# Kernel optimization log

Measured on AMD Instinct MI355X. Metric: run time of the kernel, lower is better.

The kernel has to match this reference:

```python
import jax, jax.numpy as jnp
import numpy as np

B = 16          # frames in batch
N = 16384       # atoms (num_nodes)
R = 1024        # residues (segments)
D = 320         # input_dim
BINS = 32       # adaptive-pool feature bins (output_size_per_segment[1])
H = 512         # mlp_hidden_dim
COND = 3        # conditioner dim (X_ref)
EPS = 1e-5


def setup_inputs() -> dict:
    key = jax.random.key(0)
    ks = jax.random.split(key, 8)
    x = jax.random.normal(ks[0], (B * N, D), dtype=jnp.float32)
    cond = jax.random.normal(ks[1], (N, COND), dtype=jnp.float32)
    # sorted residue ids -> contiguous variable-size segments, like real residues
    seg_ids = jnp.sort(jax.random.randint(ks[2], (N,), 0, R, dtype=jnp.int32))
    W1 = jax.random.normal(ks[3], (BINS + COND, H), dtype=jnp.float32) * 0.05
    b1 = jnp.zeros((H,), jnp.float32)
    gamma = jnp.ones((H,), jnp.float32)
    beta = jnp.zeros((H,), jnp.float32)
    bn_mean = jnp.zeros((H,), jnp.float32)
    bn_var = jnp.ones((H,), jnp.float32)
    W2 = jax.random.normal(ks[4], (H, 3), dtype=jnp.float32) * 0.05
    b2 = jnp.zeros((3,), jnp.float32)
    return {"x": x, "cond": cond, "seg_ids": seg_ids, "W1": W1, "b1": b1,
            "gamma": gamma, "beta": beta, "bn_mean": bn_mean, "bn_var": bn_var,
            "W2": W2, "b2": b2}


def reference(x, cond, seg_ids, W1, b1, gamma, beta, bn_mean, bn_var, W2, b2):
    # x: [B*N, D] atom embeddings
    x3 = x.reshape(B, N, D)
    # --- per-residue AdaptiveAvgPool2d((1, BINS)) as a fused segment mean ---
    # output height 1 == mean over all atoms of the residue
    counts = jax.ops.segment_sum(jnp.ones((N,), x.dtype), seg_ids, num_segments=R)
    sums = jax.vmap(lambda xb: jax.ops.segment_sum(xb, seg_ids, num_segments=R))(x3)  # [B,R,D]
    seg_mean = sums / jnp.maximum(counts, 1.0)[None, :, None]
    # adaptive width D -> BINS (D divisible by BINS => exact chunk means)
    pooled = seg_mean.reshape(B, R, BINS, D // BINS).mean(-1)  # [B,R,BINS]
    # --- broadcast residue feature back to atoms, concat conditioner ---
    per_atom = pooled[:, seg_ids, :]                           # [B,N,BINS]
    cond_b = jnp.broadcast_to(cond[None], (B, N, COND))
    feat = jnp.concatenate([per_atom, cond_b], axis=-1).reshape(B * N, BINS + COND)
    # --- decoder MLP: Linear -> ReLU -> BatchNorm1d(eval) -> Linear ---
    h = jnp.maximum(feat @ W1 + b1, 0.0)
    h = (h - bn_mean) * jax.lax.rsqrt(bn_var + EPS) * gamma + beta
    out = h @ W2 + b2                                          # [B*N, 3]
    return out
```

## Files before the change

### kernel.cpp

```cpp
#include <hip/hip_runtime.h>
#include <math.h>

#define B_ 16
#define N_ 16384
#define R_ 1024
#define D_ 320
#define BINS_ 32
#define H_ 512
#define EPS_ 1e-5f
#define AP 516
#define EP 260

__global__ void k_segoff(const int* __restrict__ seg, int* __restrict__ off){
  int g = blockIdx.x * blockDim.x + threadIdx.x;
  if (g > R_) return;
  int lo = 0, hi = N_;
  while (lo < hi){ int mid = (lo + hi) >> 1; if (seg[mid] < g) lo = mid + 1; else hi = mid; }
  off[g] = lo;
}

__global__ __launch_bounds__(512) void k_fold(const float* __restrict__ gamma, const float* __restrict__ beta,
                       const float* __restrict__ mean, const float* __restrict__ var,
                       const float* __restrict__ W2, const float* __restrict__ b2,
                       float* __restrict__ W2f, float* __restrict__ bias3){
  __shared__ float red[3 * H_];
  int h = threadIdx.x;
  float c = gamma[h] / sqrtf(var[h] + EPS_);
  float d = beta[h] - mean[h] * c;
  #pragma unroll
  for (int j = 0; j < 3; j++){
    float w = W2[h * 3 + j];
    W2f[h * 3 + j] = c * w;
    red[j * H_ + h] = d * w;
  }
  __syncthreads();
  for (int s = H_ / 2; s > 0; s >>= 1){
    if (h < s){
      #pragma unroll
      for (int j = 0; j < 3; j++) red[j * H_ + h] += red[j * H_ + h + s];
    }
    __syncthreads();
  }
  if (h < 3) bias3[h] = b2[h] + red[h * H_];
}

__global__ __launch_bounds__(320) void k_pool(const float* __restrict__ x, const int* __restrict__ off,
                                              float* __restrict__ pooled){
  int r = blockIdx.x, b = blockIdx.y;
  int s = off[r], e = off[r + 1];
  __shared__ float lds[D_];
  float acc = 0.f;
  const float* xp = x + ((size_t)b * N_) * D_ + threadIdx.x;
  for (int i = s; i < e; i++) acc += xp[(size_t)i * D_];
  lds[threadIdx.x] = acc;
  __syncthreads();
  if (threadIdx.x < BINS_){
    float ssum = 0.f;
    #pragma unroll
    for (int j = 0; j < 10; j++) ssum += lds[threadIdx.x * 10 + j];
    int cnt = e - s;
    float scale = 1.0f / (float)((cnt > 0 ? cnt : 1) * 10);
    pooled[((size_t)(b * R_ + r)) * BINS_ + threadIdx.x] = ssum * scale;
  }
}

__global__ __launch_bounds__(256) void k_main(const float* __restrict__ pooled, const float* __restrict__ cond,
                      const float* __restrict__ W1, const float* __restrict__ b1,
                      const int* __restrict__ off, const float* __restrict__ W2f,
                      const float* __restrict__ bias3, float* __restrict__ out){
  __shared__ __align__(16) float P[B_ * BINS_];
  __shared__ __align__(16) float A[B_ * AP];
  __shared__ __align__(16) float E[16 * EP];
  __shared__ float condT[16 * 3];
  int tid = threadIdx.x;
  int r = blockIdx.x;
  int s = off[r];
  int cnt = off[r + 1] - s;
  if (cnt == 0) return;

  for (int i = tid; i < B_ * BINS_; i += 256)
    P[i] = pooled[(size_t)((i >> 5) * R_ + r) * BINS_ + (i & 31)];
  __syncthreads();

  for (int h = tid; h < H_; h += 256){
    float bb = b1[h];
    float acc[B_];
    #pragma unroll
    for (int b = 0; b < B_; b++) acc[b] = bb;
    #pragma unroll
    for (int k = 0; k < BINS_; k++){
      float w = W1[k * H_ + h];
      #pragma unroll
      for (int b = 0; b < B_; b++) acc[b] += P[b * BINS_ + k] * w;
    }
    #pragma unroll
    for (int b = 0; b < B_; b++) A[b * AP + h] = acc[b];
  }

  int a = tid >> 4, b = tid & 15;
  for (int t0 = 0; t0 < cnt; t0 += 16){
    int na = min(16, cnt - t0);
    __syncthreads();
    if (tid < 48){
      int aa = tid / 3, c = tid % 3;
      condT[tid] = (aa < na) ? cond[(size_t)(s + t0 + aa) * 3 + c] : 0.f;
    }
    __syncthreads();
    float o0 = 0.f, o1 = 0.f, o2 = 0.f;
    int ae = a < na ? a : 0;
    for (int hc = 0; hc < 2; hc++){
      int h = (hc << 8) + tid;
      float w0 = W1[32 * H_ + h], w1 = W1[33 * H_ + h], w2 = W1[34 * H_ + h];
      for (int aa = 0; aa < na; aa++)
        E[aa * EP + tid] = condT[aa * 3] * w0 + condT[aa * 3 + 1] * w1 + condT[aa * 3 + 2] * w2;
      __syncthreads();
      const float* Ap = &A[b * AP + (hc << 8)];
      const float* Ep = &E[ae * EP];
      const float* Wp = &W2f[(hc << 8) * 3];
      #pragma unroll 4
      for (int hp = 0; hp < 256; hp += 4){
        float4 av = *(const float4*)(Ap + hp);
        float4 ev = *(const float4*)(Ep + hp);
        const float* w = Wp + hp * 3;
        float z;
        z = av.x + ev.x; z = fmaxf(z, 0.f); o0 = fmaf(z, w[0], o0); o1 = fmaf(z, w[1], o1); o2 = fmaf(z, w[2], o2);
        z = av.y + ev.y; z = fmaxf(z, 0.f); o0 = fmaf(z, w[3], o0); o1 = fmaf(z, w[4], o1); o2 = fmaf(z, w[5], o2);
        z = av.z + ev.z; z = fmaxf(z, 0.f); o0 = fmaf(z, w[6], o0); o1 = fmaf(z, w[7], o1); o2 = fmaf(z, w[8], o2);
        z = av.w + ev.w; z = fmaxf(z, 0.f); o0 = fmaf(z, w[9], o0); o1 = fmaf(z, w[10], o1); o2 = fmaf(z, w[11], o2);
      }
      __syncthreads();
    }
    if (a < na){
      size_t oi = ((size_t)b * N_ + (size_t)(s + t0 + a)) * 3;
      out[oi + 0] = o0 + bias3[0];
      out[oi + 1] = o1 + bias3[1];
      out[oi + 2] = o2 + bias3[2];
    }
  }
}

extern "C" void kernel_launch(void* const* d_in, const int* in_sizes, int n_in,
                              void* d_out, int out_size, void* d_ws, size_t ws_size,
                              hipStream_t stream) {
  const float* x      = (const float*)d_in[0];
  const float* cond   = (const float*)d_in[1];
  const int*   seg    = (const int*)  d_in[2];
  const float* W1     = (const float*)d_in[3];
  const float* b1     = (const float*)d_in[4];
  const float* gamma  = (const float*)d_in[5];
  const float* beta   = (const float*)d_in[6];
  const float* bnmean = (const float*)d_in[7];
  const float* bnvar  = (const float*)d_in[8];
  const float* W2     = (const float*)d_in[9];
  const float* b2     = (const float*)d_in[10];
  float* out = (float*)d_out;

  char* ws = (char*)d_ws;
  int*   seg_off = (int*)ws;
  float* W2f     = (float*)(ws + 8192);
  float* bias3   = (float*)(ws + 14592);
  float* pooled  = (float*)(ws + 16384);

  k_segoff<<<dim3(5), dim3(256), 0, stream>>>(seg, seg_off);
  k_fold<<<dim3(1), dim3(512), 0, stream>>>(gamma, beta, bnmean, bnvar, W2, b2, W2f, bias3);
  k_pool<<<dim3(R_, B_), dim3(320), 0, stream>>>(x, seg_off, pooled);
  k_main<<<dim3(R_), dim3(256), 0, stream>>>(pooled, cond, W1, b1, seg_off, W2f, bias3, out);
}
```

Before: 673.9 us.

## Pool over fixed atom chunks with atomic segment sums and merge prep kernels

```diff
diff --git a/kernel.cpp b/kernel.cpp
--- a/kernel.cpp
+++ b/kernel.cpp
@@ -11,56 +11,83 @@
 #define AP 516
 #define EP 260
 
-__global__ void k_segoff(const int* __restrict__ seg, int* __restrict__ off){
-  int g = blockIdx.x * blockDim.x + threadIdx.x;
-  if (g > R_) return;
-  int lo = 0, hi = N_;
-  while (lo < hi){ int mid = (lo + hi) >> 1; if (seg[mid] < g) lo = mid + 1; else hi = mid; }
-  off[g] = lo;
+__global__ __launch_bounds__(256) void k_prep(const int* __restrict__ seg,
+                      const float* __restrict__ gamma, const float* __restrict__ beta,
+                      const float* __restrict__ mean, const float* __restrict__ var,
+                      const float* __restrict__ W2, const float* __restrict__ b2,
+                      int* __restrict__ off, float* __restrict__ W2f,
+                      float* __restrict__ bias3, float* __restrict__ pooled){
+  __shared__ float red[3 * 256];
+  int blk = blockIdx.x, tid = threadIdx.x;
+  if (blk < 5){
+    int g = blk * 256 + tid;
+    if (g <= R_){
+      int lo = 0, hi = N_;
+      while (lo < hi){ int mid = (lo + hi) >> 1; if (seg[mid] < g) lo = mid + 1; else hi = mid; }
+      off[g] = lo;
+    }
+  } else if (blk == 5){
+    float p0 = 0.f, p1 = 0.f, p2 = 0.f;
+    for (int h = tid; h < H_; h += 256){
+      float c = gamma[h] / sqrtf(var[h] + EPS_);
+      float d = beta[h] - mean[h] * c;
+      float w0 = W2[h * 3 + 0], w1 = W2[h * 3 + 1], w2 = W2[h * 3 + 2];
+      W2f[h * 3 + 0] = c * w0; W2f[h * 3 + 1] = c * w1; W2f[h * 3 + 2] = c * w2;
+      p0 += d * w0; p1 += d * w1; p2 += d * w2;
+    }
+    red[tid] = p0; red[256 + tid] = p1; red[512 + tid] = p2;
+    __syncthreads();
+    for (int s = 128; s > 0; s >>= 1){
+      if (tid < s){
+        red[tid] += red[tid + s];
+        red[256 + tid] += red[256 + tid + s];
+        red[512 + tid] += red[512 + tid + s];
+      }
+      __syncthreads();
+    }
+    if (tid < 3) bias3[tid] = b2[tid] + red[tid * 256];
+  } else {
+    float4 z = {0.f, 0.f, 0.f, 0.f};
+    float4* p4 = (float4*)pooled;
+    const int total4 = B_ * R_ * BINS_ / 4;
+    for (int i = (blk - 6) * 256 + tid; i < total4; i += 32 * 256) p4[i] = z;
+  }
 }
 
-__global__ __launch_bounds__(512) void k_fold(const float* __restrict__ gamma, const float* __restrict__ beta,
-                       const float* __restrict__ mean, const float* __restrict__ var,
-                       const float* __restrict__ W2, const float* __restrict__ b2,
-                       float* __restrict__ W2f, float* __restrict__ bias3){
-  __shared__ float red[3 * H_];
-  int h = threadIdx.x;
-  float c = gamma[h] / sqrtf(var[h] + EPS_);
-  float d = beta[h] - mean[h] * c;
-  #pragma unroll
-  for (int j = 0; j < 3; j++){
-    float w = W2[h * 3 + j];
-    W2f[h * 3 + j] = c * w;
-    red[j * H_ + h] = d * w;
-  }
+__global__ __launch_bounds__(320) void k_pool(const float* __restrict__ x,
+                                              const int* __restrict__ seg,
+                                              float* __restrict__ pooled){
+  __shared__ int sseg[64];
+  __shared__ __align__(16) float red2[4 * 320];
+  int c = blockIdx.x, b = blockIdx.y, tid = threadIdx.x;
+  int base = c * 64;
+  if (tid < 64) sseg[tid] = seg[base + tid];
   __syncthreads();
-  for (int s = H_ / 2; s > 0; s >>= 1){
-    if (h < s){
+  int rowoff = tid / 80;
+  int col4 = tid - rowoff * 80;
+  const float4* xp = (const float4*)x + ((size_t)b * N_ + base) * 80 + col4;
+  int i = 0;
+  while (i < 64){
+    int sg = sseg[i];
+    int e = i + 1;
+    while (e < 64 && sseg[e] == sg) e++;
+    float4 acc = {0.f, 0.f, 0.f, 0.f};
+    for (int r = i + rowoff; r < e; r += 4){
+      float4 v = xp[(size_t)r * 80];
+      acc.x += v.x; acc.y += v.y; acc.z += v.z; acc.w += v.w;
+    }
+    *(float4*)&red2[rowoff * 320 + col4 * 4] = acc;
+    __syncthreads();
+    if (tid < 32){
+      float s = 0.f;
       #pragma unroll
-      for (int j = 0; j < 3; j++) red[j * H_ + h] += red[j * H_ + h + s];
+      for (int ro = 0; ro < 4; ro++)
+        #pragma unroll
+        for (int j = 0; j < 10; j++) s += red2[ro * 320 + tid * 10 + j];
+      atomicAdd(&pooled[((size_t)b * R_ + sg) * BINS_ + tid], s);
     }
     __syncthreads();
-  }
-  if (h < 3) bias3[h] = b2[h] + red[h * H_];
-}
-
-__global__ __launch_bounds__(320) void k_pool(const float* __restrict__ x, const int* __restrict__ off,
-                                              float* __restrict__ pooled){
-  int r = blockIdx.x, b = blockIdx.y;
-  int s = off[r], e = off[r + 1];
-  __shared__ float lds[D_];
-  float acc = 0.f;
-  const float* xp = x + ((size_t)b * N_) * D_ + threadIdx.x;
-  for (int i = s; i < e; i++) acc += xp[(size_t)i * D_];
-  lds[threadIdx.x] = acc;
-  __syncthreads();
-  if (threadIdx.x < BINS_){
-    float ssum = 0.f;
-    #pragma unroll
-    for (int j = 0; j < 10; j++) ssum += lds[threadIdx.x * 10 + j];
-    int cnt = e - s;
-    float scale = 1.0f / (float)((cnt > 0 ? cnt : 1) * 10);
-    pooled[((size_t)(b * R_ + r)) * BINS_ + threadIdx.x] = ssum * scale;
+    i = e;
   }
 }
 
@@ -78,8 +105,9 @@
   int cnt = off[r + 1] - s;
   if (cnt == 0) return;
 
+  float sc = 1.0f / (float)(cnt * 10);
   for (int i = tid; i < B_ * BINS_; i += 256)
-    P[i] = pooled[(size_t)((i >> 5) * R_ + r) * BINS_ + (i & 31)];
+    P[i] = pooled[(size_t)((i >> 5) * R_ + r) * BINS_ + (i & 31)] * sc;
   __syncthreads();
 
   for (int h = tid; h < H_; h += 256){
@@ -102,8 +130,8 @@
     int na = min(16, cnt - t0);
     __syncthreads();
     if (tid < 48){
-      int aa = tid / 3, c = tid % 3;
-      condT[tid] = (aa < na) ? cond[(size_t)(s + t0 + aa) * 3 + c] : 0.f;
+      int aa = tid / 3, cc = tid % 3;
+      condT[tid] = (aa < na) ? cond[(size_t)(s + t0 + aa) * 3 + cc] : 0.f;
     }
     __syncthreads();
     float o0 = 0.f, o1 = 0.f, o2 = 0.f;
@@ -161,8 +189,8 @@
   float* bias3   = (float*)(ws + 14592);
   float* pooled  = (float*)(ws + 16384);
 
-  k_segoff<<<dim3(5), dim3(256), 0, stream>>>(seg, seg_off);
-  k_fold<<<dim3(1), dim3(512), 0, stream>>>(gamma, beta, bnmean, bnvar, W2, b2, W2f, bias3);
-  k_pool<<<dim3(R_, B_), dim3(320), 0, stream>>>(x, seg_off, pooled);
+  k_prep<<<dim3(38), dim3(256), 0, stream>>>(seg, gamma, beta, bnmean, bnvar, W2, b2,
+                                             seg_off, W2f, bias3, pooled);
+  k_pool<<<dim3(N_ / 64, B_), dim3(320), 0, stream>>>(x, seg, pooled);
   k_main<<<dim3(R_), dim3(256), 0, stream>>>(pooled, cond, W1, b1, seg_off, W2f, bias3, out);
 }
```

After: 638.8 us. 5.2% less time.
